# Kernel optimization log

Measured on AMD Instinct MI355X. Metric: run time of the kernel, lower is better.

Reference implementation:

```python
import jax, jax.numpy as jnp
import numpy as np
from jax import lax

B, T, C = 256, 128, 512
HID, HOR = 1024, 96
THR = 1.0


def setup_inputs() -> dict:
    key = jax.random.key(0)
    ks = jax.random.split(key, 6)
    x = jax.random.normal(ks[0], (B, T, C), dtype=jnp.float32)
    # fc1: Linear(C -> HID), PyTorch layout [out, in]
    W1 = jax.random.normal(ks[1], (HID, C), dtype=jnp.float32) / np.sqrt(C)
    b1 = jax.random.normal(ks[2], (HID,), dtype=jnp.float32) * 0.01
    # head: Linear(HID -> HOR)
    Wh = jax.random.normal(ks[3], (HOR, HID), dtype=jnp.float32) / np.sqrt(HID)
    bh = jax.random.normal(ks[4], (HOR,), dtype=jnp.float32) * 0.01
    beta = jnp.float32(0.9)  # learnable leak (snntorch Leaky, learn_beta=True)
    return {"x": x, "W1": W1, "b1": b1, "Wh": Wh, "bh": bh, "beta": beta}


def reference(x, W1, b1, Wh, bh, beta):
    # Precompute all fc1 projections as one batched GEMM: [B,T,HID]
    proj = jnp.einsum("btc,hc->bth", x, W1) + b1
    beta_c = jnp.clip(beta, 0.0, 1.0)

    def step(mem, inp):
        # snntorch Leaky, reset_mechanism='subtract': reset based on PREVIOUS mem
        reset = (mem > THR).astype(mem.dtype)  # detached in snntorch
        mem_new = beta_c * mem + inp - reset * THR
        return mem_new, None

    mem0 = jnp.zeros((x.shape[0], W1.shape[0]), dtype=x.dtype)
    mem_T, _ = lax.scan(step, mem0, jnp.moveaxis(proj, 1, 0))  # scan over T
    return mem_T @ Wh.T + bh  # [B, HOR]
```

## Files before the change

### kernel.cpp

```cpp
#include <hip/hip_runtime.h>

#define TT 128
#define CC 512
#define HIDN 1024
#define HORN 96
#define NB 256
#define BN 128
#define BK 64
#define NSTAGE 8

typedef _Float16 f16x8 __attribute__((ext_vector_type(8)));
typedef _Float16 f16x4 __attribute__((ext_vector_type(4)));
typedef float f32x16 __attribute__((ext_vector_type(16)));

#define XHI 0
#define XLO 16384
#define WHI 32768
#define WLO 49152
#define SMEM_BYTES 65536

__device__ __forceinline__ void cvt_split(const float4 v, f16x4* hi, f16x4* lo) {
    auto h01 = __builtin_amdgcn_cvt_pkrtz(v.x, v.y);
    auto h23 = __builtin_amdgcn_cvt_pkrtz(v.z, v.w);
    auto l01 = __builtin_amdgcn_cvt_pkrtz(v.x - (float)h01.x, v.y - (float)h01.y);
    auto l23 = __builtin_amdgcn_cvt_pkrtz(v.z - (float)h23.x, v.w - (float)h23.y);
    *hi = (f16x4){(_Float16)h01.x, (_Float16)h01.y, (_Float16)h23.x, (_Float16)h23.y};
    *lo = (f16x4){(_Float16)l01.x, (_Float16)l01.y, (_Float16)l23.x, (_Float16)l23.y};
}

__device__ __forceinline__ void gload16(const void* g, void* l) {
    __builtin_amdgcn_global_load_lds(
        (const __attribute__((address_space(1))) unsigned int*)g,
        (__attribute__((address_space(3))) unsigned int*)l, 16, 0, 0);
}

__global__ void __launch_bounds__(256)
snn_cvtw(const float* __restrict__ W1, f16x4* __restrict__ whi, f16x4* __restrict__ wlo)
{
    const int i = blockIdx.x * 256 + threadIdx.x;
    const float4 v = ((const float4*)W1)[i];
    f16x4 hi, lo;
    cvt_split(v, &hi, &lo);
    whi[i] = hi;
    wlo[i] = lo;
}

__global__ void __launch_bounds__(256, 2)
snn_proj_scan(const float* __restrict__ x, const _Float16* __restrict__ whi_g,
              const _Float16* __restrict__ wlo_g, const float* __restrict__ b1,
              const float* __restrict__ betap, float* __restrict__ memT)
{
    __shared__ __align__(16) char smem[SMEM_BYTES];

    const int tid  = threadIdx.x;
    const int lane = tid & 63;
    const int wid  = tid >> 6;
    const int wm = wid >> 1, wn = wid & 1;
    const int g2 = lane >> 5, lr = lane & 31;

    const int lid  = blockIdx.x;
    const int slot = lid >> 3;
    const int b     = ((lid & 7) << 5) + (slot >> 3);
    const int hbase = (slot & 7) * BN;

    const float* __restrict__ xg = x + (size_t)b * TT * CC;

    const int srow = tid >> 4;
    const int skq  = tid & 15;
    const float* xrow = xg + srow * CC + skq * 4;
    const int wbyte = (skq * 8) ^ ((srow & 7) << 4);

    const int wrow0  = lane >> 3;
    const int wslotb = ((lane & 7) ^ wrow0) * 16;
    const char* whsrc = (const char*)whi_g + ((size_t)(hbase + wrow0) * CC) * 2 + wslotb;
    const char* wlsrc = (const char*)wlo_g + ((size_t)(hbase + wrow0) * CC) * 2 + wslotb;

    const int sw    = (lr & 7) << 4;
    const int arow0 = (wm * 64 +  0 + lr) * 128;
    const int arow1 = (wm * 64 + 32 + lr) * 128;
    const int brow0 = (wn * 64 +  0 + lr) * 128;
    const int brow1 = (wn * 64 + 32 + lr) * 128;

    f32x16 acc00 = {}, acc01 = {}, acc10 = {}, acc11 = {};

    float4 px[8];
#pragma unroll
    for (int p = 0; p < 8; ++p) px[p] = *(const float4*)(xrow + p * 16 * CC);

    for (int s = 0; s < NSTAGE; ++s) {
#pragma unroll
        for (int c = 0; c < 4; ++c) {
            const int chunk = wid * 4 + c;
            const size_t go = (size_t)chunk * (8 * CC * 2) + (size_t)s * (BK * 2);
            gload16(whsrc + go, smem + WHI + chunk * 1024);
            gload16(wlsrc + go, smem + WLO + chunk * 1024);
        }
#pragma unroll
        for (int p = 0; p < 8; ++p) {
            const int byte = (srow + 16 * p) * 128 + wbyte;
            f16x4 hi, lo;
            cvt_split(px[p], &hi, &lo);
            *(f16x4*)(smem + XHI + byte) = hi;
            *(f16x4*)(smem + XLO + byte) = lo;
        }
        __syncthreads();

        if (s + 1 < NSTAGE) {
            const int ko = (s + 1) * BK;
#pragma unroll
            for (int p = 0; p < 8; ++p)
                px[p] = *(const float4*)(xrow + p * 16 * CC + ko);
        }

#pragma unroll
        for (int ks = 0; ks < 4; ++ks) {
            const int off = ((ks << 5) | (g2 << 4)) ^ sw;
            const f16x8 ah0 = *(const f16x8*)(smem + XHI + arow0 + off);
            const f16x8 ah1 = *(const f16x8*)(smem + XHI + arow1 + off);
            const f16x8 al0 = *(const f16x8*)(smem + XLO + arow0 + off);
            const f16x8 al1 = *(const f16x8*)(smem + XLO + arow1 + off);
            const f16x8 bh0 = *(const f16x8*)(smem + WHI + brow0 + off);
            const f16x8 bh1 = *(const f16x8*)(smem + WHI + brow1 + off);
            const f16x8 bl0 = *(const f16x8*)(smem + WLO + brow0 + off);
            const f16x8 bl1 = *(const f16x8*)(smem + WLO + brow1 + off);

            acc00 = __builtin_amdgcn_mfma_f32_32x32x16_f16(ah0, bh0, acc00, 0, 0, 0);
            acc00 = __builtin_amdgcn_mfma_f32_32x32x16_f16(ah0, bl0, acc00, 0, 0, 0);
            acc00 = __builtin_amdgcn_mfma_f32_32x32x16_f16(al0, bh0, acc00, 0, 0, 0);

            acc01 = __builtin_amdgcn_mfma_f32_32x32x16_f16(ah0, bh1, acc01, 0, 0, 0);
            acc01 = __builtin_amdgcn_mfma_f32_32x32x16_f16(ah0, bl1, acc01, 0, 0, 0);
            acc01 = __builtin_amdgcn_mfma_f32_32x32x16_f16(al0, bh1, acc01, 0, 0, 0);

            acc10 = __builtin_amdgcn_mfma_f32_32x32x16_f16(ah1, bh0, acc10, 0, 0, 0);
            acc10 = __builtin_amdgcn_mfma_f32_32x32x16_f16(ah1, bl0, acc10, 0, 0, 0);
            acc10 = __builtin_amdgcn_mfma_f32_32x32x16_f16(al1, bh0, acc10, 0, 0, 0);

            acc11 = __builtin_amdgcn_mfma_f32_32x32x16_f16(ah1, bh1, acc11, 0, 0, 0);
            acc11 = __builtin_amdgcn_mfma_f32_32x32x16_f16(ah1, bl1, acc11, 0, 0, 0);
            acc11 = __builtin_amdgcn_mfma_f32_32x32x16_f16(al1, bh1, acc11, 0, 0, 0);
        }
        __syncthreads();
    }

#define ST_ACC(A, m, n) {                                                        \
        const int row   = wn * 64 + (n) * 32 + lr;                               \
        const int sbase = wm * 16 + (m) * 8 + g2;                                \
        const int rs    = row & 31;                                              \
        char* rb = smem + row * 512;                                             \
        *(float4*)(rb + (((sbase + 0) ^ rs) * 16)) = make_float4(A[0],  A[1],  A[2],  A[3]);  \
        *(float4*)(rb + (((sbase + 2) ^ rs) * 16)) = make_float4(A[4],  A[5],  A[6],  A[7]);  \
        *(float4*)(rb + (((sbase + 4) ^ rs) * 16)) = make_float4(A[8],  A[9],  A[10], A[11]); \
        *(float4*)(rb + (((sbase + 6) ^ rs) * 16)) = make_float4(A[12], A[13], A[14], A[15]); }
    ST_ACC(acc00, 0, 0)
    ST_ACC(acc01, 0, 1)
    ST_ACC(acc10, 1, 0)
    ST_ACC(acc11, 1, 1)
#undef ST_ACC
    __syncthreads();

    if (tid < BN) {
        const float beta_c = fminf(fmaxf(betap[0], 0.0f), 1.0f);
        const float b1h = b1[hbase + tid];
        const char* rb = smem + tid * 512;
        const int rs = tid & 31;
        float mem = 0.0f;
#pragma unroll
        for (int q = 0; q < 32; ++q) {
            const float4 v = *(const float4*)(rb + ((q ^ rs) * 16));
            float reset;
            reset = (mem > 1.0f) ? 1.0f : 0.0f; mem = beta_c * mem + (v.x + b1h) - reset;
            reset = (mem > 1.0f) ? 1.0f : 0.0f; mem = beta_c * mem + (v.y + b1h) - reset;
            reset = (mem > 1.0f) ? 1.0f : 0.0f; mem = beta_c * mem + (v.z + b1h) - reset;
            reset = (mem > 1.0f) ? 1.0f : 0.0f; mem = beta_c * mem + (v.w + b1h) - reset;
        }
        memT[(size_t)b * HIDN + hbase + tid] = mem;
    }
}

__global__ void __launch_bounds__(256)
snn_head(const float* __restrict__ memT, const float* __restrict__ Wh,
         const float* __restrict__ bh, float* __restrict__ out)
{
    __shared__ __align__(16) float ms[HIDN];
    const int b   = blockIdx.x;
    const int tid = threadIdx.x;
    ((float4*)ms)[tid] = ((const float4*)(memT + (size_t)b * HIDN))[tid];
    __syncthreads();

    const int lane = tid & 63, wid = tid >> 6;
    for (int o = wid; o < HORN; o += 4) {
        const float4* wr = (const float4*)(Wh + (size_t)o * HIDN);
        float a = 0.0f;
#pragma unroll
        for (int q = 0; q < 4; ++q) {
            const float4 w = wr[q * 64 + lane];
            const float4 m = ((const float4*)ms)[q * 64 + lane];
            a = fmaf(w.x, m.x, fmaf(w.y, m.y, fmaf(w.z, m.z, fmaf(w.w, m.w, a))));
        }
#pragma unroll
        for (int d = 32; d; d >>= 1) a += __shfl_xor(a, d);
        if (lane == 0) out[(size_t)b * HORN + o] = a + bh[o];
    }
}

extern "C" void kernel_launch(void* const* d_in, const int* in_sizes, int n_in,
                              void* d_out, int out_size, void* d_ws, size_t ws_size,
                              hipStream_t stream)
{
    (void)in_sizes; (void)n_in; (void)out_size; (void)ws_size;
    const float* x    = (const float*)d_in[0];
    const float* W1   = (const float*)d_in[1];
    const float* b1   = (const float*)d_in[2];
    const float* Wh   = (const float*)d_in[3];
    const float* bh   = (const float*)d_in[4];
    const float* beta = (const float*)d_in[5];

    char* ws = (char*)d_ws;
    _Float16* whi = (_Float16*)(ws);
    _Float16* wlo = (_Float16*)(ws + (1 << 20));
    float*    memT = (float*)(ws + (2 << 20));

    snn_cvtw<<<512, 256, 0, stream>>>(W1, (f16x4*)whi, (f16x4*)wlo);
    snn_proj_scan<<<2048, 256, 0, stream>>>(x, whi, wlo, b1, beta, memT);
    snn_head<<<NB, 256, 0, stream>>>(memT, Wh, bh, (float*)d_out);
}
```

Before: 213.2 us.

## Double-buffer MFMA fragments with setprio and split head GEMV across K chunks

The main GEMM inner loop now preloads LDS fragments for two k-steps, alternates loads and MFMA groups, and raises wave priority around the MFMA block so LDS reads hide behind matrix math. MFMAs are also reordered so the four accumulators are interleaved, which shortens dependent chains. The head kernel becomes a 16x16 grid: each block handles one 64-wide K chunk for 16 batch rows and accumulates into the output with atomicAdd. The bias is pre-written into the output by the weight conversion kernel. This trades more register pressure and non-deterministic atomic summation for better latency hiding and more head parallelism.

```diff
diff --git a/kernel.cpp b/kernel.cpp
--- a/kernel.cpp
+++ b/kernel.cpp
@@ -35,7 +35,8 @@
 }
 
 __global__ void __launch_bounds__(256)
-snn_cvtw(const float* __restrict__ W1, f16x4* __restrict__ whi, f16x4* __restrict__ wlo)
+snn_cvtw(const float* __restrict__ W1, f16x4* __restrict__ whi, f16x4* __restrict__ wlo,
+         const float* __restrict__ bh, float* __restrict__ out)
 {
     const int i = blockIdx.x * 256 + threadIdx.x;
     const float4 v = ((const float4*)W1)[i];
@@ -43,6 +44,7 @@
     cvt_split(v, &hi, &lo);
     whi[i] = hi;
     wlo[i] = lo;
+    if (i < NB * HORN) out[i] = bh[i % HORN];
 }
 
 __global__ void __launch_bounds__(256, 2)
@@ -86,6 +88,31 @@
     float4 px[8];
 #pragma unroll
     for (int p = 0; p < 8; ++p) px[p] = *(const float4*)(xrow + p * 16 * CC);
+
+#define FRAG_SET(P) f16x8 ah0##P, ah1##P, al0##P, al1##P, bh0##P, bh1##P, bl0##P, bl1##P;
+#define FRAG_LOAD(P, KS) { \
+        const int off = (((KS) << 5) | (g2 << 4)) ^ sw; \
+        ah0##P = *(const f16x8*)(smem + XHI + arow0 + off); \
+        ah1##P = *(const f16x8*)(smem + XHI + arow1 + off); \
+        al0##P = *(const f16x8*)(smem + XLO + arow0 + off); \
+        al1##P = *(const f16x8*)(smem + XLO + arow1 + off); \
+        bh0##P = *(const f16x8*)(smem + WHI + brow0 + off); \
+        bh1##P = *(const f16x8*)(smem + WHI + brow1 + off); \
+        bl0##P = *(const f16x8*)(smem + WLO + brow0 + off); \
+        bl1##P = *(const f16x8*)(smem + WLO + brow1 + off); }
+#define FRAG_MFMA(P) \
+        acc00 = __builtin_amdgcn_mfma_f32_32x32x16_f16(ah0##P, bh0##P, acc00, 0, 0, 0); \
+        acc01 = __builtin_amdgcn_mfma_f32_32x32x16_f16(ah0##P, bh1##P, acc01, 0, 0, 0); \
+        acc10 = __builtin_amdgcn_mfma_f32_32x32x16_f16(ah1##P, bh0##P, acc10, 0, 0, 0); \
+        acc11 = __builtin_amdgcn_mfma_f32_32x32x16_f16(ah1##P, bh1##P, acc11, 0, 0, 0); \
+        acc00 = __builtin_amdgcn_mfma_f32_32x32x16_f16(ah0##P, bl0##P, acc00, 0, 0, 0); \
+        acc01 = __builtin_amdgcn_mfma_f32_32x32x16_f16(ah0##P, bl1##P, acc01, 0, 0, 0); \
+        acc10 = __builtin_amdgcn_mfma_f32_32x32x16_f16(ah1##P, bl0##P, acc10, 0, 0, 0); \
+        acc11 = __builtin_amdgcn_mfma_f32_32x32x16_f16(ah1##P, bl1##P, acc11, 0, 0, 0); \
+        acc00 = __builtin_amdgcn_mfma_f32_32x32x16_f16(al0##P, bh0##P, acc00, 0, 0, 0); \
+        acc01 = __builtin_amdgcn_mfma_f32_32x32x16_f16(al0##P, bh1##P, acc01, 0, 0, 0); \
+        acc10 = __builtin_amdgcn_mfma_f32_32x32x16_f16(al1##P, bh0##P, acc10, 0, 0, 0); \
+        acc11 = __builtin_amdgcn_mfma_f32_32x32x16_f16(al1##P, bh1##P, acc11, 0, 0, 0);
 
     for (int s = 0; s < NSTAGE; ++s) {
 #pragma unroll
@@ -112,36 +139,25 @@
                 px[p] = *(const float4*)(xrow + p * 16 * CC + ko);
         }
 
-#pragma unroll
-        for (int ks = 0; ks < 4; ++ks) {
-            const int off = ((ks << 5) | (g2 << 4)) ^ sw;
-            const f16x8 ah0 = *(const f16x8*)(smem + XHI + arow0 + off);
-            const f16x8 ah1 = *(const f16x8*)(smem + XHI + arow1 + off);
-            const f16x8 al0 = *(const f16x8*)(smem + XLO + arow0 + off);
-            const f16x8 al1 = *(const f16x8*)(smem + XLO + arow1 + off);
-            const f16x8 bh0 = *(const f16x8*)(smem + WHI + brow0 + off);
-            const f16x8 bh1 = *(const f16x8*)(smem + WHI + brow1 + off);
-            const f16x8 bl0 = *(const f16x8*)(smem + WLO + brow0 + off);
-            const f16x8 bl1 = *(const f16x8*)(smem + WLO + brow1 + off);
-
-            acc00 = __builtin_amdgcn_mfma_f32_32x32x16_f16(ah0, bh0, acc00, 0, 0, 0);
-            acc00 = __builtin_amdgcn_mfma_f32_32x32x16_f16(ah0, bl0, acc00, 0, 0, 0);
-            acc00 = __builtin_amdgcn_mfma_f32_32x32x16_f16(al0, bh0, acc00, 0, 0, 0);
-
-            acc01 = __builtin_amdgcn_mfma_f32_32x32x16_f16(ah0, bh1, acc01, 0, 0, 0);
-            acc01 = __builtin_amdgcn_mfma_f32_32x32x16_f16(ah0, bl1, acc01, 0, 0, 0);
-            acc01 = __builtin_amdgcn_mfma_f32_32x32x16_f16(al0, bh1, acc01, 0, 0, 0);
-
-            acc10 = __builtin_amdgcn_mfma_f32_32x32x16_f16(ah1, bh0, acc10, 0, 0, 0);
-            acc10 = __builtin_amdgcn_mfma_f32_32x32x16_f16(ah1, bl0, acc10, 0, 0, 0);
-            acc10 = __builtin_amdgcn_mfma_f32_32x32x16_f16(al1, bh0, acc10, 0, 0, 0);
-
-            acc11 = __builtin_amdgcn_mfma_f32_32x32x16_f16(ah1, bh1, acc11, 0, 0, 0);
-            acc11 = __builtin_amdgcn_mfma_f32_32x32x16_f16(ah1, bl1, acc11, 0, 0, 0);
-            acc11 = __builtin_amdgcn_mfma_f32_32x32x16_f16(al1, bh1, acc11, 0, 0, 0);
+        {
+            FRAG_SET(A)
+            FRAG_SET(B)
+            FRAG_LOAD(A, 0)
+            FRAG_LOAD(B, 1)
+            __builtin_amdgcn_s_setprio(1);
+            FRAG_MFMA(A)
+            FRAG_LOAD(A, 2)
+            FRAG_MFMA(B)
+            FRAG_LOAD(B, 3)
+            FRAG_MFMA(A)
+            FRAG_MFMA(B)
+            __builtin_amdgcn_s_setprio(0);
         }
         __syncthreads();
     }
+#undef FRAG_SET
+#undef FRAG_LOAD
+#undef FRAG_MFMA
 
 #define ST_ACC(A, m, n) {                                                        \
         const int row   = wn * 64 + (n) * 32 + lr;                               \
@@ -180,27 +196,42 @@
 
 __global__ void __launch_bounds__(256)
 snn_head(const float* __restrict__ memT, const float* __restrict__ Wh,
-         const float* __restrict__ bh, float* __restrict__ out)
-{
-    __shared__ __align__(16) float ms[HIDN];
-    const int b   = blockIdx.x;
+         float* __restrict__ out)
+{
+    __shared__ __align__(16) float ms[16][64];
+    __shared__ __align__(16) float ws[HORN][64];
     const int tid = threadIdx.x;
-    ((float4*)ms)[tid] = ((const float4*)(memT + (size_t)b * HIDN))[tid];
+    const int kc = blockIdx.x, bg = blockIdx.y;
+    const int kof = kc * 64;
+
+    {
+        const int row = tid >> 4, c4 = tid & 15;
+        *(float4*)&ms[row][c4 * 4] =
+            *(const float4*)(memT + (size_t)(bg * 16 + row) * HIDN + kof + c4 * 4);
+    }
+#pragma unroll
+    for (int r = 0; r < 6; ++r) {
+        const int q = r * 256 + tid;
+        const int row = q >> 4, c4 = q & 15;
+        *(float4*)&ws[row][c4 * 4] =
+            *(const float4*)(Wh + (size_t)row * HIDN + kof + c4 * 4);
+    }
     __syncthreads();
 
-    const int lane = tid & 63, wid = tid >> 6;
-    for (int o = wid; o < HORN; o += 4) {
-        const float4* wr = (const float4*)(Wh + (size_t)o * HIDN);
+#pragma unroll
+    for (int r = 0; r < 6; ++r) {
+        const int p = r * 256 + tid;
+        const int bb = p / HORN, o = p % HORN;
+        const float4* mv = (const float4*)&ms[bb][0];
+        const float4* wv = (const float4*)&ws[o][0];
         float a = 0.0f;
 #pragma unroll
-        for (int q = 0; q < 4; ++q) {
-            const float4 w = wr[q * 64 + lane];
-            const float4 m = ((const float4*)ms)[q * 64 + lane];
+        for (int q = 0; q < 16; ++q) {
+            const float4 w = wv[q];
+            const float4 m = mv[q];
             a = fmaf(w.x, m.x, fmaf(w.y, m.y, fmaf(w.z, m.z, fmaf(w.w, m.w, a))));
         }
-#pragma unroll
-        for (int d = 32; d; d >>= 1) a += __shfl_xor(a, d);
-        if (lane == 0) out[(size_t)b * HORN + o] = a + bh[o];
+        atomicAdd(out + (size_t)(bg * 16 + bb) * HORN + o, a);
     }
 }
 
@@ -220,8 +251,9 @@
     _Float16* whi = (_Float16*)(ws);
     _Float16* wlo = (_Float16*)(ws + (1 << 20));
     float*    memT = (float*)(ws + (2 << 20));
-
-    snn_cvtw<<<512, 256, 0, stream>>>(W1, (f16x4*)whi, (f16x4*)wlo);
+    float*    out  = (float*)d_out;
+
+    snn_cvtw<<<512, 256, 0, stream>>>(W1, (f16x4*)whi, (f16x4*)wlo, bh, out);
     snn_proj_scan<<<2048, 256, 0, stream>>>(x, whi, wlo, b1, beta, memT);
-    snn_head<<<NB, 256, 0, stream>>>(memT, Wh, bh, (float*)d_out);
-}
+    snn_head<<<dim3(16, 16), 256, 0, stream>>>(memT, Wh, out);
+}
```

Measured after the change: 212.4 us. No clear change (-0.4%).
